# Performance work log

Measured on AMD Instinct MI355X. Metric: run time of the kernel, lower is better.

## Reference

```python
import jax, jax.numpy as jnp
import numpy as np

B, N, FIN, T = 4, 10000, 1, 12
K, CF, FT, H, NH = 3, 64, 64, 2, 4
E = 160000


def setup_inputs() -> dict:
    key = jax.random.key(0)
    ks = jax.random.split(key, 16)
    s = 0.05
    return {
        'x': jax.random.normal(ks[0], (B, N, FIN, T), jnp.float32),
        'edge_index': jax.random.randint(ks[1], (2, E), 0, N, jnp.int32),
        'cheb_w': jax.random.normal(ks[2], (K, CF, FIN), jnp.float32) * s,
        'cheb_b': jnp.zeros((CF,), jnp.float32),
        'gat_w': jax.random.normal(ks[3], (H * CF, CF), jnp.float32) * s,
        'att_src': jax.random.normal(ks[4], (H, CF), jnp.float32) * s,
        'att_dst': jax.random.normal(ks[5], (H, CF), jnp.float32) * s,
        'gat_b': jnp.zeros((CF,), jnp.float32),
        'tc_w': jax.random.normal(ks[6], (FT, CF, 1, 3), jnp.float32) * s,
        'tc_b': jnp.zeros((FT,), jnp.float32),
        'in_w': jax.random.normal(ks[7], (3 * FT, FT), jnp.float32) * s,
        'in_b': jnp.zeros((3 * FT,), jnp.float32),
        'out_w': jax.random.normal(ks[8], (FT, FT), jnp.float32) * s,
        'out_b': jnp.zeros((FT,), jnp.float32),
        'res_w': jax.random.normal(ks[9], (FT, FIN, 1, 1), jnp.float32) * s,
        'res_b': jnp.zeros((FT,), jnp.float32),
        'ln_g': jnp.ones((FT,), jnp.float32),
        'ln_b': jnp.zeros((FT,), jnp.float32),
        'bc_w': jax.random.normal(ks[10], (FT, CF, 1, 3), jnp.float32) * s,
        'bc_b': jnp.zeros((FT,), jnp.float32),
        'fc_w': jax.random.normal(ks[11], (FT, CF, 1, 3), jnp.float32) * s,
        'fc_b': jnp.zeros((FT,), jnp.float32),
    }


def conv1x3(inp, w, b):
    # Conv2d kernel (1,3), stride 1, pad (0,1) over (B,C,N,T): 1D conv along time.
    out = jax.lax.conv_general_dilated(inp, w, (1, 1), ((0, 0), (1, 1)),
                                       dimension_numbers=('NCHW', 'OIHW', 'NCHW'))
    return out + b[None, :, None, None]


def reference(x, edge_index, cheb_w, cheb_b, gat_w, att_src, att_dst, gat_b,
              tc_w, tc_b, in_w, in_b, out_w, out_b, res_w, res_b, ln_g, ln_b,
              bc_w, bc_b, fc_w, fc_b):
    Bx, Nx, Fin, Tt = x.shape
    BN = Bx * Nx
    src, dst = edge_index[0], edge_index[1]
    # ChebConv norm (PyG, lambda_max=2, sym): L_hat = -D^{-1/2} A D^{-1/2}, zero diag
    deg = jax.ops.segment_sum(jnp.ones_like(src, jnp.float32), src, num_segments=BN)
    dis = jnp.where(deg > 0, deg ** -0.5, 0.0)
    w_e = -dis[src] * dis[dst]
    loops = jnp.arange(BN, dtype=src.dtype)
    src_g = jnp.concatenate([src, loops])
    dst_g = jnp.concatenate([dst, loops])

    def prop(v):  # v: (BN, F) -> L_hat @ v
        return jax.ops.segment_sum(w_e[:, None] * v[src], dst, num_segments=BN)

    def spatial(xt):  # xt: (BN, Fin) -> (BN, CF); ChebConv then GAT (eval, no dropout)
        Tx0 = xt
        out = Tx0 @ cheb_w[0].T
        Tx1 = prop(Tx0)
        out = out + Tx1 @ cheb_w[1].T
        for kk in range(2, K):
            Tx2 = 2.0 * prop(Tx1) - Tx0
            out = out + Tx2 @ cheb_w[kk].T
            Tx0, Tx1 = Tx1, Tx2
        h = out + cheb_b
        # GATConv: heads=H, concat=False, self-loops added for all BN nodes
        xp = (h @ gat_w.T).reshape(BN, H, CF)
        a_s = (xp * att_src).sum(-1)  # (BN,H)
        a_d = (xp * att_dst).sum(-1)
        e = jax.nn.leaky_relu(a_s[src_g] + a_d[dst_g], 0.2)  # (E+BN,H)
        m = jax.ops.segment_max(e, dst_g, num_segments=BN)
        p = jnp.exp(e - m[dst_g])
        z = jax.ops.segment_sum(p, dst_g, num_segments=BN)
        alpha = p / z[dst_g]
        agg = jax.ops.segment_sum(alpha[:, :, None] * xp[src_g], dst_g, num_segments=BN)
        return agg.mean(1) + gat_b

    # batch graph convs across timesteps
    x_t = x.transpose(3, 0, 1, 2).reshape(Tt, BN, Fin)
    sp = jax.vmap(spatial)(x_t)  # (T,BN,CF)
    spatial_out = sp.reshape(Tt, Bx, Nx, CF).transpose(1, 3, 2, 0)  # (B,CF,N,T)

    tc = conv1x3(spatial_out, tc_w, tc_b)  # (B,FT,N,T)
    temp_in = tc.transpose(0, 2, 3, 1).reshape(BN, Tt, FT)
    # MultiheadAttention (batch_first, 4 heads, eval)
    qkv = temp_in @ in_w.T + in_b
    q, k, v = jnp.split(qkv, 3, axis=-1)
    dh = FT // NH
    q = q.reshape(BN, Tt, NH, dh)
    k = k.reshape(BN, Tt, NH, dh)
    v = v.reshape(BN, Tt, NH, dh)
    sc = jnp.einsum('bqhd,bkhd->bhqk', q, k) / jnp.sqrt(jnp.float32(dh))
    a = jax.nn.softmax(sc, axis=-1)
    o = jnp.einsum('bhqk,bkhd->bqhd', a, v).reshape(BN, Tt, FT)
    attn = o @ out_w.T + out_b
    temp_out = attn.reshape(Bx, Nx, Tt, FT).transpose(0, 1, 3, 2)  # (B,N,FT,T)

    # residual 1x1 conv (stride 1)
    x_res = jnp.einsum('bnft,of->bnot', x, res_w[:, :, 0, 0]) + res_b[None, None, :, None]
    zr = jax.nn.relu(x_res + temp_out)  # (B,N,FT,T)
    mu = zr.mean(axis=2, keepdims=True)
    var = ((zr - mu) ** 2).mean(axis=2, keepdims=True)
    result = (zr - mu) * jax.lax.rsqrt(var + 1e-5) * ln_g[None, None, :, None] + ln_b[None, None, :, None]

    rp = result.transpose(0, 2, 1, 3)  # (B,FT,N,T)
    backcast = conv1x3(rp, bc_w, bc_b).transpose(0, 2, 1, 3)
    forecast = conv1x3(rp, fc_w, fc_b).transpose(0, 2, 1, 3)
    return (backcast, forecast)
```

## Files before the change

kernel.cpp:

```cpp
#include <hip/hip_runtime.h>

#define BN 40000
#define TT 12
#define EE 160000

typedef __attribute__((ext_vector_type(4))) float f32x4;
typedef __attribute__((ext_vector_type(4))) short s16x4;
typedef __attribute__((ext_vector_type(8))) short s16x8;

__device__ __forceinline__ float lrelu(float v){ return v > 0.f ? v : 0.2f*v; }

__device__ __forceinline__ short bf(float f){
  union { float f; unsigned u; } x; x.f = f;
  unsigned r = x.u + 0x7fffu + ((x.u >> 16) & 1u);
  return (short)(r >> 16);
}

__device__ __forceinline__ unsigned cvtpk(float lo, float hi){
  unsigned r;
  asm("v_cvt_pk_bf16_f32 %0, %1, %2" : "=v"(r) : "v"(lo), "v"(hi));
  return r;
}

__global__ void k_histprep(const int* __restrict__ ei, int* __restrict__ degcnt, int* __restrict__ cnt,
                       const float* __restrict__ cheb_w, const float* __restrict__ cheb_b,
                       const float* __restrict__ gat_w, const float* __restrict__ att_src,
                       const float* __restrict__ att_dst, const float* __restrict__ gat_b,
                       const float* __restrict__ tc_w, const float* __restrict__ tc_b,
                       const float* __restrict__ in_w, const float* __restrict__ out_w,
                       const float* __restrict__ bc_w, const float* __restrict__ fc_w,
                       float* __restrict__ gwbuf, short* __restrict__ wp, float* __restrict__ btcT){
  if (blockIdx.x < 625){
    int e = blockIdx.x*256 + threadIdx.x;
    if (e < EE){
      atomicAdd(&degcnt[ei[e]], 1);
      atomicAdd(&cnt[ei[EE + e]], 1);
    }
    return;
  }
  if (blockIdx.x == 625){
    __shared__ float sgw[384]; __shared__ float sgc[128];
    int hc = threadIdx.x;
    if (hc < 128){
      for (int k=0;k<3;++k){
        float a=0; for (int c=0;c<64;++c) a += cheb_w[k*64+c]*gat_w[hc*64+c];
        sgw[k*128+hc]=a; gwbuf[k*128+hc]=a;
      }
      float g=0; for (int c=0;c<64;++c) g += cheb_b[c]*gat_w[hc*64+c];
      sgc[hc]=g; gwbuf[384+hc]=g;
    }
    __syncthreads();
    if (hc<6){ int k=hc>>1, h=hc&1; float a=0,d=0;
      for (int c=0;c<64;++c){ float g=sgw[k*128+h*64+c]; a+=g*att_src[h*64+c]; d+=g*att_dst[h*64+c]; }
      gwbuf[512+hc]=a; gwbuf[518+hc]=d; }
    if (hc<2){ float a=0,d=0;
      for (int c=0;c<64;++c){ float g=sgc[hc*64+c]; a+=g*att_src[hc*64+c]; d+=g*att_dst[hc*64+c]; }
      gwbuf[524+hc]=a; gwbuf[526+hc]=d; }
    __syncthreads();
    if (hc < 64){
      int o = hc;
      short* gw2 = wp + 46080;
      float sbias[3];
      for (int dt=0; dt<3; ++dt){
        float s[6] = {0,0,0,0,0,0};
        float sb = 0.f;
        for (int c=0;c<64;++c){
          float wv = tc_w[o*192 + c*3 + dt];
          for (int j=0;j<3;++j){
            s[j]   += wv * sgw[j*128 + c];
            s[3+j] += wv * sgw[j*128 + 64 + c];
          }
          sb += wv * (gat_b[c] + 0.5f*(sgc[c] + sgc[64+c]));
        }
        for (int j=0;j<6;++j) gw2[o*40 + dt*6 + j] = bf(s[j]);
        sbias[dt] = sb;
      }
      for (int k=18;k<40;++k) gw2[o*40+k] = 0;
      for (int t=0;t<16;++t){
        float b = tc_b[o];
        if (t < 12){
          if (t > 0)  b += sbias[0];
          b += sbias[1];
          if (t < 11) b += sbias[2];
        }
        btcT[o*16+t] = b;
      }
    }
    return;
  }
  int i = (blockIdx.x-626)*256 + threadIdx.x;
  if (i >= 46080) return;
  float v;
  if (i < 13824){ int j=i/72, k=i%72; v = (k<64)? in_w[j*64+k] : 0.f; }
  else if (i < 27648){ int d=i-13824; int dt=d/4608, rr=d%4608, o=rr/72, c=rr%72; v = (c<64)? bc_w[o*192+c*3+dt] : 0.f; }
  else if (i < 41472){ int d=i-27648; int dt=d/4608, rr=d%4608, o=rr/72, c=rr%72; v = (c<64)? fc_w[o*192+c*3+dt] : 0.f; }
  else               { int d=i-41472; int o=d/72, c=d%72; v = (c<64)? out_w[o*64+c] : 0.f; }
  wp[i] = bf(v);
}

__global__ void k_scanA(const int* __restrict__ cnt, int* __restrict__ bsum,
                        const short* __restrict__ wp, short* __restrict__ wp2){
  if (blockIdx.x >= 157){
    int i = (blockIdx.x-157)*256 + threadIdx.x;
    if (i >= 40960) return;
    int f2 = i >> 9, lane = (i >> 3) & 63, e = i & 7;
    int l15 = lane & 15, l4 = lane >> 4;
    int src;
    if (f2 < 24){
      int grp = f2 >> 3, nt = (f2 >> 1) & 3, kc = f2 & 1;
      src = 0     + ((grp*4+nt)*16 + l15)*72 + kc*32 + l4*8 + e;
    } else if (f2 < 32){
      int g = f2 - 24; int mt = g >> 1, kc = g & 1;
      src = 41472 + (mt*16 + l15)*72 + kc*32 + l4*8 + e;
    } else if (f2 < 56){
      int g = f2 - 32; int dt = g >> 3, kc = (g >> 2) & 1, nt = g & 3;
      src = 13824 + (dt*64 + nt*16 + l15)*72 + kc*32 + l4*8 + e;
    } else {
      int g = f2 - 56; int dt = g >> 3, kc = (g >> 2) & 1, nt = g & 3;
      src = 27648 + (dt*64 + nt*16 + l15)*72 + kc*32 + l4*8 + e;
    }
    wp2[i] = wp[src];
    return;
  }
  __shared__ int s[256];
  int i = blockIdx.x*256 + threadIdx.x;
  int v = (i < BN) ? cnt[i] : 0;
  s[threadIdx.x] = v; __syncthreads();
  for (int off=128; off>0; off>>=1){
    if (threadIdx.x < off) s[threadIdx.x] += s[threadIdx.x+off];
    __syncthreads();
  }
  if (threadIdx.x == 0) bsum[blockIdx.x] = s[0];
}

__global__ void k_scanB(const int* __restrict__ bsum, int* __restrict__ bbase, int* __restrict__ rowptr){
  __shared__ int s[256];
  int tid = threadIdx.x;
  int v = (tid < 157) ? bsum[tid] : 0;
  s[tid] = v; __syncthreads();
  for (int off=1; off<256; off<<=1){
    int t = (tid>=off) ? s[tid-off] : 0;
    __syncthreads();
    s[tid] += t;
    __syncthreads();
  }
  if (tid < 157) bbase[tid] = s[tid] - v;
  if (tid == 0) rowptr[BN] = EE;
}

__global__ void k_scanC(const int* __restrict__ cnt, const int* __restrict__ bbase,
                        int* __restrict__ rowptr, int* __restrict__ cursor){
  __shared__ int s[256];
  int i = blockIdx.x*256 + threadIdx.x;
  int v = (i < BN) ? cnt[i] : 0;
  s[threadIdx.x] = v; __syncthreads();
  for (int off=1; off<256; off<<=1){
    int t = (threadIdx.x>=off) ? s[threadIdx.x-off] : 0;
    __syncthreads();
    s[threadIdx.x] += t;
    __syncthreads();
  }
  if (i < BN){
    int r = bbase[blockIdx.x] + s[threadIdx.x] - v;
    rowptr[i] = r; cursor[i] = r;
  }
}

__global__ void k_scatter(const int* __restrict__ ei, const int* __restrict__ degcnt,
                          int* __restrict__ cursor, int* __restrict__ esrc, float* __restrict__ ew){
  int e = blockIdx.x*256 + threadIdx.x;
  if (e < EE){
    int s = ei[e], d = ei[EE+e];
    int p = atomicAdd(&cursor[d], 1);
    esrc[p] = s;
    int ds_ = degcnt[s], dd_ = degcnt[d];
    float isd = ds_ > 0 ? rsqrtf((float)ds_) : 0.f;
    float idd = dd_ > 0 ? rsqrtf((float)dd_) : 0.f;
    ew[p] = -isd*idd;
  }
}

__global__ void k_prop1v(const float* __restrict__ x, const int* __restrict__ rowptr,
                         const int* __restrict__ esrc, const float* __restrict__ ew,
                         float* __restrict__ tx1){
  int i = blockIdx.x*256 + threadIdx.x;
  if (i >= BN*3) return;
  int d = i/3, q = i - d*3;
  int r0 = rowptr[d], r1 = rowptr[d+1];
  float4 a = {0.f,0.f,0.f,0.f};
  for (int p=r0;p<r1;++p){
    float wv = ew[p];
    float4 v = ((const float4*)x)[esrc[p]*3 + q];
    a.x += wv*v.x; a.y += wv*v.y; a.z += wv*v.z; a.w += wv*v.w;
  }
  ((float4*)tx1)[i] = a;
}

__global__ void k_prop2v(const float* __restrict__ x, const float* __restrict__ tx1,
                         const int* __restrict__ rowptr, const int* __restrict__ esrc,
                         const float* __restrict__ ew, float* __restrict__ tx2){
  int i = blockIdx.x*256 + threadIdx.x;
  if (i >= BN*3) return;
  int d = i/3, q = i - d*3;
  int r0 = rowptr[d], r1 = rowptr[d+1];
  float4 a = {0.f,0.f,0.f,0.f};
  for (int p=r0;p<r1;++p){
    float wv = ew[p];
    float4 v = ((const float4*)tx1)[esrc[p]*3 + q];
    a.x += wv*v.x; a.y += wv*v.y; a.z += wv*v.z; a.w += wv*v.w;
  }
  float4 xv = ((const float4*)x)[i];
  float4 o; o.x = 2.f*a.x - xv.x; o.y = 2.f*a.y - xv.y; o.z = 2.f*a.z - xv.z; o.w = 2.f*a.w - xv.w;
  ((float4*)tx2)[i] = o;
}

__global__ __launch_bounds__(256) void k_gat4(const float* __restrict__ x, const float* __restrict__ tx1,
     const float* __restrict__ tx2, const int* __restrict__ rowptr, const int* __restrict__ esrc,
     const float* __restrict__ gwbuf, float* __restrict__ coef, int cst){
  int i = blockIdx.x*256 + threadIdx.x;
  if (i >= BN*3) return;
  int d = i/3, q = i - d*3;

  float as[2][3], ad[2][3], asc[2], adc[2];
  #pragma unroll
  for (int h=0;h<2;++h){
    #pragma unroll
    for (int k=0;k<3;++k){ as[h][k] = gwbuf[512+2*k+h]; ad[h][k] = gwbuf[518+2*k+h]; }
    asc[h] = gwbuf[524+h]; adc[h] = gwbuf[526+h];
  }

  float4 t0 = ((const float4*)x)[d*3+q];
  float4 t1 = ((const float4*)tx1)[d*3+q];
  float4 t2 = ((const float4*)tx2)[d*3+q];
  float td0[4] = {t0.x,t0.y,t0.z,t0.w};
  float td1[4] = {t1.x,t1.y,t1.z,t1.w};
  float td2[4] = {t2.x,t2.y,t2.z,t2.w};

  float adh[2][4], S0[2][4], S1[2][4], S2[2][4], Z[2][4];
  #pragma unroll
  for (int h=0;h<2;++h){
    #pragma unroll
    for (int t=0;t<4;++t){
      adh[h][t] = td0[t]*ad[h][0] + td1[t]*ad[h][1] + td2[t]*ad[h][2] + adc[h];
      float es = lrelu(td0[t]*as[h][0] + td1[t]*as[h][1] + td2[t]*as[h][2] + asc[h] + adh[h][t]);
      float p = __expf(es);
      S0[h][t] = p*td0[t]; S1[h][t] = p*td1[t]; S2[h][t] = p*td2[t]; Z[h][t] = p;
    }
  }
  int r0 = rowptr[d], r1 = rowptr[d+1];
  for (int p=r0;p<r1;++p){
    int s = esrc[p];
    float4 v0 = ((const float4*)x)[s*3+q];
    float4 v1 = ((const float4*)tx1)[s*3+q];
    float4 v2 = ((const float4*)tx2)[s*3+q];
    float s0[4] = {v0.x,v0.y,v0.z,v0.w};
    float s1[4] = {v1.x,v1.y,v1.z,v1.w};
    float s2[4] = {v2.x,v2.y,v2.z,v2.w};
    #pragma unroll
    for (int h=0;h<2;++h){
      #pragma unroll
      for (int t=0;t<4;++t){
        float e = lrelu(s0[t]*as[h][0] + s1[t]*as[h][1] + s2[t]*as[h][2] + asc[h] + adh[h][t]);
        float pp = __expf(e);
        S0[h][t] += pp*s0[t]; S1[h][t] += pp*s1[t]; S2[h][t] += pp*s2[t]; Z[h][t] += pp;
      }
    }
  }
  float* cw = coef + (size_t)d*cst + q*32;
  #pragma unroll
  for (int t=0;t<4;++t){
    float inv0 = 0.5f/Z[0][t], inv1 = 0.5f/Z[1][t];
    float4 w4; w4.x = S0[0][t]*inv0; w4.y = S1[0][t]*inv0; w4.z = S2[0][t]*inv0; w4.w = S0[1][t]*inv1;
    *(float4*)(cw + t*8) = w4;
    float2 w2; w2.x = S1[1][t]*inv1; w2.y = S2[1][t]*inv1;
    *(float2*)(cw + t*8 + 4) = w2;
  }
}

__global__ __launch_bounds__(448) void k_temporal9(
  const float* __restrict__ coef, int cst, const float* __restrict__ x,
  const short* __restrict__ wp, const short* __restrict__ wp2, const float* __restrict__ btcT,
  const float* __restrict__ in_b, const float* __restrict__ out_b,
  const float* __restrict__ res_w, const float* __restrict__ res_b,
  const float* __restrict__ ln_g, const float* __restrict__ ln_b,
  const float* __restrict__ bc_b, const float* __restrict__ fc_b,
  float* __restrict__ out)
{
  __shared__ __align__(16) short lds[26880];

  const int tid = threadIdx.x;
  const int wv = tid >> 6;
  const int lane = tid & 63;
  const int l15 = lane & 15, l4 = lane >> 4;
  const int nd = blockIdx.x*7 + wv;
  if (nd >= BN) return;

  short* nb  = lds + wv*3840;
  short* tcO = nb;
  short* K   = nb + 1152;
  short* R   = nb + 1152;
  short* Vt  = nb + 2304;
  short* Pb  = nb + 3328;
  short* Pb2 = nb + 3584;

  const f32x4 z4 = {0.f,0.f,0.f,0.f};
  s16x8 zf;
  #pragma unroll
  for (int j=0;j<8;++j) zf[j]=0;

  s16x8 aA;
  {
    const float* cb = coef + (size_t)nd*cst;
    float av[8];
    #pragma unroll
    for (int e=0; e<8; ++e){
      int k = l4*8 + e;
      float v = 0.f;
      if (k < 18){
        int dt = (k>=12) ? 2 : ((k>=6) ? 1 : 0);
        int j = k - dt*6;
        int u = l15 - 1 + dt;
        if (u >= 0 && u < 12) v = cb[u*8 + j];
      }
      av[e] = v;
    }
    unsigned* ap = (unsigned*)&aA;
    ap[0]=cvtpk(av[0],av[1]); ap[1]=cvtpk(av[2],av[3]);
    ap[2]=cvtpk(av[4],av[5]); ap[3]=cvtpk(av[6],av[7]);
  }

  {
    #pragma unroll
    for (int nt=0; nt<4; ++nt){
      s16x8 b = *(const s16x8*)&wp[46080 + (nt*16+l15)*40 + l4*8];
      f32x4 acc = __builtin_amdgcn_mfma_f32_16x16x32_bf16(aA, b, z4, 0,0,0);
      float4 bb = *(const float4*)&btcT[(nt*16+l15)*16 + l4*4];
      unsigned p01 = cvtpk(acc[0]+bb.x, acc[1]+bb.y);
      unsigned p23 = cvtpk(acc[2]+bb.z, acc[3]+bb.w);
      int c = nt*16 + l15, rb = l4*4;
      tcO[(rb+0)*72+c] = (short)p01; tcO[(rb+1)*72+c] = (short)(p01>>16);
      tcO[(rb+2)*72+c] = (short)p23; tcO[(rb+3)*72+c] = (short)(p23>>16);
    }
  }

  {
    s16x8 a0 = *(const s16x8*)&tcO[l15*72 +  0 + l4*8];
    s16x8 a1 = *(const s16x8*)&tcO[l15*72 + 32 + l4*8];
    #pragma unroll
    for (int grp=0; grp<3; ++grp){
      f32x4 acc[4];
      #pragma unroll
      for (int nt=0; nt<4; ++nt){
        s16x8 b0 = *(const s16x8*)&wp2[(((grp*8 + nt*2 + 0)*64 + lane))*8];
        acc[nt] = __builtin_amdgcn_mfma_f32_16x16x32_bf16(a0, b0, z4, 0,0,0);
        s16x8 b1 = *(const s16x8*)&wp2[(((grp*8 + nt*2 + 1)*64 + lane))*8];
        acc[nt] = __builtin_amdgcn_mfma_f32_16x16x32_bf16(a1, b1, acc[nt], 0,0,0);
      }
      #pragma unroll
      for (int nt=0; nt<4; ++nt){
        float bb = in_b[(grp*4+nt)*16 + l15];
        unsigned p01 = cvtpk(acc[nt][0]+bb, acc[nt][1]+bb);
        unsigned p23 = cvtpk(acc[nt][2]+bb, acc[nt][3]+bb);
        if (grp==0){
          int c = nt*16+l15, rb = l4*4;
          tcO[(rb+0)*72+c] = (short)p01; tcO[(rb+1)*72+c] = (short)(p01>>16);
          tcO[(rb+2)*72+c] = (short)p23; tcO[(rb+3)*72+c] = (short)(p23>>16);
        } else if (grp==1){
          int c = nt*16+l15, rb = l4*4;
          K[(rb+0)*72+c] = (short)p01; K[(rb+1)*72+c] = (short)(p01>>16);
          K[(rb+2)*72+c] = (short)p23; K[(rb+3)*72+c] = (short)(p23>>16);
        } else {
          int2 pk2; pk2.x = (int)p01; pk2.y = (int)p23;
          *(int2*)&Vt[(nt*16 + l15)*16 + l4*4] = pk2;
        }
      }
    }
  }

  {
    #pragma unroll 1
    for (int hp=0; hp<2; ++hp){
      const int h0 = hp*2, h1 = hp*2 + 1;
      s16x8 qa0 = zf, kb0 = zf, qa1 = zf, kb1 = zf;
      if (l4 < 2){
        qa0 = *(const s16x8*)&tcO[l15*72 + h0*16 + l4*8];
        kb0 = *(const s16x8*)&K[l15*72 + h0*16 + l4*8];
        qa1 = *(const s16x8*)&tcO[l15*72 + h1*16 + l4*8];
        kb1 = *(const s16x8*)&K[l15*72 + h1*16 + l4*8];
      }
      f32x4 sc0 = __builtin_amdgcn_mfma_f32_16x16x32_bf16(qa0, kb0, z4, 0,0,0);
      f32x4 sc1 = __builtin_amdgcn_mfma_f32_16x16x32_bf16(qa1, kb1, z4, 0,0,0);
      float invz0[4], invz1[4], ev0[4], ev1[4];
      #pragma unroll
      for (int r=0; r<4; ++r){
        float e0 = (l15 < 12) ? __expf(sc0[r]*0.25f) : 0.f;
        float e1 = (l15 < 12) ? __expf(sc1[r]*0.25f) : 0.f;
        float z0 = e0, z1 = e1;
        #pragma unroll
        for (int dd=1; dd<16; dd<<=1){ z0 += __shfl_xor(z0, dd); z1 += __shfl_xor(z1, dd); }
        invz0[r] = 1.f/z0; invz1[r] = 1.f/z1;
        ev0[r] = e0; ev1[r] = e1;
      }
      {
        unsigned a01 = cvtpk(ev0[0],ev0[1]), a23 = cvtpk(ev0[2],ev0[3]);
        unsigned b01 = cvtpk(ev1[0],ev1[1]), b23 = cvtpk(ev1[2],ev1[3]);
        int rb = l4*4, c = l15;
        Pb [(rb+0)*16+c] = (short)a01; Pb [(rb+1)*16+c] = (short)(a01>>16);
        Pb [(rb+2)*16+c] = (short)a23; Pb [(rb+3)*16+c] = (short)(a23>>16);
        Pb2[(rb+0)*16+c] = (short)b01; Pb2[(rb+1)*16+c] = (short)(b01>>16);
        Pb2[(rb+2)*16+c] = (short)b23; Pb2[(rb+3)*16+c] = (short)(b23>>16);
      }
      s16x8 pa0 = zf, vb0 = zf, pa1 = zf, vb1 = zf;
      if (l4 < 2){
        pa0 = *(const s16x8*)&Pb [l15*16 + l4*8];
        vb0 = *(const s16x8*)&Vt[(h0*16 + l15)*16 + l4*8];
        pa1 = *(const s16x8*)&Pb2[l15*16 + l4*8];
        vb1 = *(const s16x8*)&Vt[(h1*16 + l15)*16 + l4*8];
      }
      f32x4 ov0 = __builtin_amdgcn_mfma_f32_16x16x32_bf16(pa0, vb0, z4, 0,0,0);
      f32x4 ov1 = __builtin_amdgcn_mfma_f32_16x16x32_bf16(pa1, vb1, z4, 0,0,0);
      {
        unsigned a01 = cvtpk(ov0[0]*invz0[0], ov0[1]*invz0[1]);
        unsigned a23 = cvtpk(ov0[2]*invz0[2], ov0[3]*invz0[3]);
        unsigned b01 = cvtpk(ov1[0]*invz1[0], ov1[1]*invz1[1]);
        unsigned b23 = cvtpk(ov1[2]*invz1[2], ov1[3]*invz1[3]);
        int c0 = h0*16 + l15, c1 = h1*16 + l15, rb = l4*4;
        tcO[(rb+0)*72+c0] = (short)a01; tcO[(rb+1)*72+c0] = (short)(a01>>16);
        tcO[(rb+2)*72+c0] = (short)a23; tcO[(rb+3)*72+c0] = (short)(a23>>16);
        tcO[(rb+0)*72+c1] = (short)b01; tcO[(rb+1)*72+c1] = (short)(b01>>16);
        tcO[(rb+2)*72+c1] = (short)b23; tcO[(rb+3)*72+c1] = (short)(b23>>16);
      }
    }
  }

  {
    s16x4 zz; zz[0]=0; zz[1]=0; zz[2]=0; zz[3]=0;
    for (int i=lane; i<108; i+=64){
      int rr = i/18, cc = i%18;
      int row = (rr==0) ? 0 : (12 + rr);
      *(s16x4*)&R[row*72 + cc*4] = zz;
    }
    s16x8 a0 = *(const s16x8*)&tcO[l15*72 +  0 + l4*8];
    s16x8 a1 = *(const s16x8*)&tcO[l15*72 + 32 + l4*8];
    f32x4 acc[4];
    #pragma unroll
    for (int nt=0; nt<4; ++nt){
      s16x8 w0 = *(const s16x8*)&wp2[(((24 + nt*2 + 0)*64 + lane))*8];
      acc[nt] = __builtin_amdgcn_mfma_f32_16x16x32_bf16(a0, w0, z4, 0,0,0);
      s16x8 w1 = *(const s16x8*)&wp2[(((24 + nt*2 + 1)*64 + lane))*8];
      acc[nt] = __builtin_amdgcn_mfma_f32_16x16x32_bf16(a1, w1, acc[nt], 0,0,0);
    }
    float4 xv = {0.f,0.f,0.f,0.f};
    if (l4 < 3) xv = *(const float4*)&x[(size_t)nd*12 + l4*4];
    float xr[4] = {xv.x, xv.y, xv.z, xv.w};
    float zr[4][4], sum[4]={0,0,0,0}, sq[4]={0,0,0,0};
    #pragma unroll
    for (int nt=0; nt<4; ++nt){
      int o = nt*16 + l15;
      float ob=out_b[o], rw=res_w[o], rb2=res_b[o];
      #pragma unroll
      for (int r=0; r<4; ++r){
        float v = acc[nt][r] + ob + xr[r]*rw + rb2;
        v = v>0.f ? v : 0.f;
        zr[nt][r]=v; sum[r]+=v; sq[r]+=v*v;
      }
    }
    #pragma unroll
    for (int r=0; r<4; ++r){
      #pragma unroll
      for (int dd=1; dd<16; dd<<=1){ sum[r]+=__shfl_xor(sum[r],dd); sq[r]+=__shfl_xor(sq[r],dd); }
    }
    if (l4 < 3){
      float mu4[4], iv4[4];
      #pragma unroll
      for (int r=0; r<4; ++r){
        float mu = sum[r]*(1.f/64.f);
        float va = sq[r]*(1.f/64.f) - mu*mu;
        mu4[r] = mu; iv4[r] = rsqrtf(fmaxf(va,0.f) + 1e-5f);
      }
      #pragma unroll
      for (int nt=0; nt<4; ++nt){
        int o = nt*16 + l15;
        float g = ln_g[o], b2 = ln_b[o];
        float r0 = (zr[nt][0]-mu4[0])*iv4[0]*g + b2;
        float r1 = (zr[nt][1]-mu4[1])*iv4[1]*g + b2;
        float r2 = (zr[nt][2]-mu4[2])*iv4[2]*g + b2;
        float r3 = (zr[nt][3]-mu4[3])*iv4[3]*g + b2;
        unsigned p01 = cvtpk(r0,r1), p23 = cvtpk(r2,r3);
        int rb = l4*4;
        R[(rb+1)*72+o] = (short)p01; R[(rb+2)*72+o] = (short)(p01>>16);
        R[(rb+3)*72+o] = (short)p23; R[(rb+4)*72+o] = (short)(p23>>16);
      }
    }
  }

  {
    f32x4 aB[4] = {z4,z4,z4,z4};
    f32x4 aF[4] = {z4,z4,z4,z4};
    #pragma unroll
    for (int dt=0; dt<3; ++dt){
      #pragma unroll
      for (int kc=0; kc<2; ++kc){
        s16x8 ar = *(const s16x8*)&R[(l15 + dt)*72 + kc*32 + l4*8];
        #pragma unroll
        for (int nt=0; nt<4; ++nt){
          s16x8 wb = *(const s16x8*)&wp2[16384 + (((dt*8 + kc*4 + nt)*64 + lane))*8];
          aB[nt] = __builtin_amdgcn_mfma_f32_16x16x32_bf16(ar, wb, aB[nt], 0,0,0);
          s16x8 wf = *(const s16x8*)&wp2[28672 + (((dt*8 + kc*4 + nt)*64 + lane))*8];
          aF[nt] = __builtin_amdgcn_mfma_f32_16x16x32_bf16(ar, wf, aF[nt], 0,0,0);
        }
      }
    }
    if (l4 < 3){
      #pragma unroll
      for (int nt=0; nt<4; ++nt){
        int o = nt*16 + l15;
        float bb = bc_b[o], fb = fc_b[o];
        float4 v; v.x=aB[nt][0]+bb; v.y=aB[nt][1]+bb; v.z=aB[nt][2]+bb; v.w=aB[nt][3]+bb;
        *(float4*)&out[(size_t)nd*768 + o*12 + l4*4] = v;
        float4 f; f.x=aF[nt][0]+fb; f.y=aF[nt][1]+fb; f.z=aF[nt][2]+fb; f.w=aF[nt][3]+fb;
        *(float4*)&out[30720000 + (size_t)nd*768 + o*12 + l4*4] = f;
      }
    }
  }
}

extern "C" void kernel_launch(void* const* d_in, const int* in_sizes, int n_in,
                              void* d_out, int out_size, void* d_ws, size_t ws_size,
                              hipStream_t stream){
  const float* x      = (const float*)d_in[0];
  const int*   ei     = (const int*)d_in[1];
  const float* cheb_w = (const float*)d_in[2];
  const float* cheb_b = (const float*)d_in[3];
  const float* gat_w  = (const float*)d_in[4];
  const float* att_src= (const float*)d_in[5];
  const float* att_dst= (const float*)d_in[6];
  const float* gat_b  = (const float*)d_in[7];
  const float* tc_w   = (const float*)d_in[8];
  const float* tc_b   = (const float*)d_in[9];
  const float* in_w   = (const float*)d_in[10];
  const float* in_b   = (const float*)d_in[11];
  const float* out_w  = (const float*)d_in[12];
  const float* out_b  = (const float*)d_in[13];
  const float* res_w  = (const float*)d_in[14];
  const float* res_b  = (const float*)d_in[15];
  const float* ln_g   = (const float*)d_in[16];
  const float* ln_b   = (const float*)d_in[17];
  const float* bc_w   = (const float*)d_in[18];
  const float* bc_b   = (const float*)d_in[19];
  const float* fc_w   = (const float*)d_in[20];
  const float* fc_b   = (const float*)d_in[21];
  float* out = (float*)d_out;

  char* w = (char*)d_ws;
  size_t off = 0;
  auto alloc = [&](size_t bytes)->void*{ void* p = w + off; off += (bytes + 255) & ~(size_t)255; return p; };
  int*   cnt2   = (int*)alloc((size_t)2*BN*4);
  int*   degcnt = cnt2;
  int*   cnt    = cnt2 + BN;
  int*   rowptr = (int*)alloc((size_t)(BN+1)*4);
  int*   cursor = (int*)alloc((size_t)BN*4);
  int*   esrc   = (int*)alloc((size_t)EE*4);
  float* ew     = (float*)alloc((size_t)EE*4);
  float* tx1    = (float*)alloc((size_t)BN*TT*4);
  float* tx2    = (float*)alloc((size_t)BN*TT*4);
  float* gwb    = (float*)alloc(1024*4);
  short* wpack  = (short*)alloc((size_t)48640*2);
  short* wpack2 = (short*)alloc((size_t)40960*2);
  float* btcT   = (float*)alloc(1024*4);
  int*   bsum   = (int*)alloc(157*4);
  int*   bbase  = (int*)alloc(157*4);

  size_t coefBytes = (size_t)BN*TT*8*4;
  float* coefp; int cst;
  if (off + coefBytes <= ws_size){ coefp = (float*)(w + off); off += coefBytes; cst = 96; }
  else { coefp = out; cst = 768; }

  hipMemsetAsync(cnt2, 0, (size_t)2*BN*4, stream);
  k_histprep<<<806, 256, 0, stream>>>(ei, degcnt, cnt, cheb_w, cheb_b, gat_w, att_src, att_dst,
                                      gat_b, tc_w, tc_b, in_w, out_w, bc_w, fc_w, gwb, wpack, btcT);
  k_scanA   <<<317, 256, 0, stream>>>(cnt, bsum, wpack, wpack2);
  k_scanB   <<<1, 256, 0, stream>>>(bsum, bbase, rowptr);
  k_scanC   <<<157, 256, 0, stream>>>(cnt, bbase, rowptr, cursor);
  k_scatter <<<(EE+255)/256, 256, 0, stream>>>(ei, degcnt, cursor, esrc, ew);
  k_prop1v  <<<(BN*3+255)/256, 256, 0, stream>>>(x, rowptr, esrc, ew, tx1);
  k_prop2v  <<<(BN*3+255)/256, 256, 0, stream>>>(x, tx1, rowptr, esrc, ew, tx2);
  k_gat4    <<<(BN*3+255)/256, 256, 0, stream>>>(x, tx1, tx2, rowptr, esrc, gwb, coefp, cst);
  k_temporal9<<<(BN+6)/7, 448, 0, stream>>>(coefp, cst, x, wpack, wpack2, btcT, in_b, out_b,
                                            res_w, res_b, ln_g, ln_b, bc_b, fc_b, out);
}
```

Baseline: 266.1 us.

## Fold temporal conv into QKV projection and interleave Chebyshev features for gather

Precomputes the product of the in_proj weights with the folded GAT/temporal-conv weights (and the matching biases) in the prep block, so the temporal kernel computes Q/K/V with a single K=32 MFMA per tile instead of a conv followed by a two-step K=64 projection. It also packs x, Tx1 and Tx2 into one interleaved 48-byte record per node-quarter, so each neighbor gather in the GAT kernel reads one contiguous record instead of three separate arrays. In exchange, one prep block does more serial work, weight rounding to bf16 now happens after the fold, and the propagation kernel writes a larger packed buffer.

Result: slower. 306.3 us (+15.1%).

```diff
diff --git a/kernel.cpp b/kernel.cpp
--- a/kernel.cpp
+++ b/kernel.cpp
@@ -27,9 +27,10 @@
                        const float* __restrict__ gat_w, const float* __restrict__ att_src,
                        const float* __restrict__ att_dst, const float* __restrict__ gat_b,
                        const float* __restrict__ tc_w, const float* __restrict__ tc_b,
-                       const float* __restrict__ in_w, const float* __restrict__ out_w,
+                       const float* __restrict__ in_w, const float* __restrict__ in_b,
+                       const float* __restrict__ out_w,
                        const float* __restrict__ bc_w, const float* __restrict__ fc_w,
-                       float* __restrict__ gwbuf, short* __restrict__ wp, float* __restrict__ btcT){
+                       float* __restrict__ gwbuf, short* __restrict__ wp, float* __restrict__ bbT){
   if (blockIdx.x < 625){
     int e = blockIdx.x*256 + threadIdx.x;
     if (e < EE){
@@ -40,6 +41,7 @@
   }
   if (blockIdx.x == 625){
     __shared__ float sgw[384]; __shared__ float sgc[128];
+    __shared__ float gwtcF[64*18]; __shared__ float btcF[16*64];
     int hc = threadIdx.x;
     if (hc < 128){
       for (int k=0;k<3;++k){
@@ -72,7 +74,10 @@
           }
           sb += wv * (gat_b[c] + 0.5f*(sgc[c] + sgc[64+c]));
         }
-        for (int j=0;j<6;++j) gw2[o*40 + dt*6 + j] = bf(s[j]);
+        for (int j=0;j<6;++j){
+          gw2[o*40 + dt*6 + j] = bf(s[j]);
+          gwtcF[o*18 + dt*6 + j] = s[j];
+        }
         sbias[dt] = sb;
       }
       for (int k=18;k<40;++k) gw2[o*40+k] = 0;
@@ -83,7 +88,25 @@
           b += sbias[1];
           if (t < 11) b += sbias[2];
         }
-        btcT[o*16+t] = b;
+        btcF[t*64+o] = b;
+      }
+    }
+    __syncthreads();
+    if (hc < 192){
+      int j = hc;
+      float wrow[64];
+      for (int o=0;o<64;++o) wrow[o] = in_w[j*64+o];
+      short* wbq = wp + 48640;
+      for (int k=0;k<18;++k){
+        float a = 0.f;
+        for (int o=0;o<64;++o) a += wrow[o]*gwtcF[o*18+k];
+        wbq[j*32+k] = bf(a);
+      }
+      for (int k=18;k<32;++k) wbq[j*32+k] = 0;
+      for (int t=0;t<16;++t){
+        float a = in_b[j];
+        for (int o=0;o<64;++o) a += wrow[o]*btcF[t*64+o];
+        bbT[j*16+t] = a;
       }
     }
     return;
@@ -196,9 +219,9 @@
   ((float4*)tx1)[i] = a;
 }
 
-__global__ void k_prop2v(const float* __restrict__ x, const float* __restrict__ tx1,
+__global__ void k_prop2p(const float* __restrict__ x, const float* __restrict__ tx1,
                          const int* __restrict__ rowptr, const int* __restrict__ esrc,
-                         const float* __restrict__ ew, float* __restrict__ tx2){
+                         const float* __restrict__ ew, float* __restrict__ pk){
   int i = blockIdx.x*256 + threadIdx.x;
   if (i >= BN*3) return;
   int d = i/3, q = i - d*3;
@@ -210,12 +233,16 @@
     a.x += wv*v.x; a.y += wv*v.y; a.z += wv*v.z; a.w += wv*v.w;
   }
   float4 xv = ((const float4*)x)[i];
+  float4 t1o = ((const float4*)tx1)[i];
   float4 o; o.x = 2.f*a.x - xv.x; o.y = 2.f*a.y - xv.y; o.z = 2.f*a.z - xv.z; o.w = 2.f*a.w - xv.w;
-  ((float4*)tx2)[i] = o;
-}
-
-__global__ __launch_bounds__(256) void k_gat4(const float* __restrict__ x, const float* __restrict__ tx1,
-     const float* __restrict__ tx2, const int* __restrict__ rowptr, const int* __restrict__ esrc,
+  float* base = pk + (size_t)i*12;
+  *(float4*)(base+0) = xv;
+  *(float4*)(base+4) = t1o;
+  *(float4*)(base+8) = o;
+}
+
+__global__ __launch_bounds__(256) void k_gat5(const float* __restrict__ pk,
+     const int* __restrict__ rowptr, const int* __restrict__ esrc,
      const float* __restrict__ gwbuf, float* __restrict__ coef, int cst){
   int i = blockIdx.x*256 + threadIdx.x;
   if (i >= BN*3) return;
@@ -229,9 +256,10 @@
     asc[h] = gwbuf[524+h]; adc[h] = gwbuf[526+h];
   }
 
-  float4 t0 = ((const float4*)x)[d*3+q];
-  float4 t1 = ((const float4*)tx1)[d*3+q];
-  float4 t2 = ((const float4*)tx2)[d*3+q];
+  const float* bd = pk + (size_t)i*12;
+  float4 t0 = *(const float4*)(bd+0);
+  float4 t1 = *(const float4*)(bd+4);
+  float4 t2 = *(const float4*)(bd+8);
   float td0[4] = {t0.x,t0.y,t0.z,t0.w};
   float td1[4] = {t1.x,t1.y,t1.z,t1.w};
   float td2[4] = {t2.x,t2.y,t2.z,t2.w};
@@ -250,9 +278,10 @@
   int r0 = rowptr[d], r1 = rowptr[d+1];
   for (int p=r0;p<r1;++p){
     int s = esrc[p];
-    float4 v0 = ((const float4*)x)[s*3+q];
-    float4 v1 = ((const float4*)tx1)[s*3+q];
-    float4 v2 = ((const float4*)tx2)[s*3+q];
+    const float* bs = pk + (size_t)(s*3+q)*12;
+    float4 v0 = *(const float4*)(bs+0);
+    float4 v1 = *(const float4*)(bs+4);
+    float4 v2 = *(const float4*)(bs+8);
     float s0[4] = {v0.x,v0.y,v0.z,v0.w};
     float s1[4] = {v1.x,v1.y,v1.z,v1.w};
     float s2[4] = {v2.x,v2.y,v2.z,v2.w};
@@ -277,11 +306,10 @@
   }
 }
 
-__global__ __launch_bounds__(448) void k_temporal9(
+__global__ __launch_bounds__(448) void k_temporalA(
   const float* __restrict__ coef, int cst, const float* __restrict__ x,
-  const short* __restrict__ wp, const short* __restrict__ wp2, const float* __restrict__ btcT,
-  const float* __restrict__ in_b, const float* __restrict__ out_b,
-  const float* __restrict__ res_w, const float* __restrict__ res_b,
+  const short* __restrict__ wp, const short* __restrict__ wp2, const float* __restrict__ bbT,
+  const float* __restrict__ out_b, const float* __restrict__ res_w, const float* __restrict__ res_b,
   const float* __restrict__ ln_g, const float* __restrict__ ln_b,
   const float* __restrict__ bc_b, const float* __restrict__ fc_b,
   float* __restrict__ out)
@@ -332,48 +360,35 @@
   {
     #pragma unroll
     for (int nt=0; nt<4; ++nt){
-      s16x8 b = *(const s16x8*)&wp[46080 + (nt*16+l15)*40 + l4*8];
+      s16x8 b = *(const s16x8*)&wp[48640 + (nt*16+l15)*32 + l4*8];
       f32x4 acc = __builtin_amdgcn_mfma_f32_16x16x32_bf16(aA, b, z4, 0,0,0);
-      float4 bb = *(const float4*)&btcT[(nt*16+l15)*16 + l4*4];
+      float4 bb = *(const float4*)&bbT[(nt*16+l15)*16 + l4*4];
       unsigned p01 = cvtpk(acc[0]+bb.x, acc[1]+bb.y);
       unsigned p23 = cvtpk(acc[2]+bb.z, acc[3]+bb.w);
       int c = nt*16 + l15, rb = l4*4;
       tcO[(rb+0)*72+c] = (short)p01; tcO[(rb+1)*72+c] = (short)(p01>>16);
       tcO[(rb+2)*72+c] = (short)p23; tcO[(rb+3)*72+c] = (short)(p23>>16);
     }
-  }
-
-  {
-    s16x8 a0 = *(const s16x8*)&tcO[l15*72 +  0 + l4*8];
-    s16x8 a1 = *(const s16x8*)&tcO[l15*72 + 32 + l4*8];
-    #pragma unroll
-    for (int grp=0; grp<3; ++grp){
-      f32x4 acc[4];
-      #pragma unroll
-      for (int nt=0; nt<4; ++nt){
-        s16x8 b0 = *(const s16x8*)&wp2[(((grp*8 + nt*2 + 0)*64 + lane))*8];
-        acc[nt] = __builtin_amdgcn_mfma_f32_16x16x32_bf16(a0, b0, z4, 0,0,0);
-        s16x8 b1 = *(const s16x8*)&wp2[(((grp*8 + nt*2 + 1)*64 + lane))*8];
-        acc[nt] = __builtin_amdgcn_mfma_f32_16x16x32_bf16(a1, b1, acc[nt], 0,0,0);
-      }
-      #pragma unroll
-      for (int nt=0; nt<4; ++nt){
-        float bb = in_b[(grp*4+nt)*16 + l15];
-        unsigned p01 = cvtpk(acc[nt][0]+bb, acc[nt][1]+bb);
-        unsigned p23 = cvtpk(acc[nt][2]+bb, acc[nt][3]+bb);
-        if (grp==0){
-          int c = nt*16+l15, rb = l4*4;
-          tcO[(rb+0)*72+c] = (short)p01; tcO[(rb+1)*72+c] = (short)(p01>>16);
-          tcO[(rb+2)*72+c] = (short)p23; tcO[(rb+3)*72+c] = (short)(p23>>16);
-        } else if (grp==1){
-          int c = nt*16+l15, rb = l4*4;
-          K[(rb+0)*72+c] = (short)p01; K[(rb+1)*72+c] = (short)(p01>>16);
-          K[(rb+2)*72+c] = (short)p23; K[(rb+3)*72+c] = (short)(p23>>16);
-        } else {
-          int2 pk2; pk2.x = (int)p01; pk2.y = (int)p23;
-          *(int2*)&Vt[(nt*16 + l15)*16 + l4*4] = pk2;
-        }
-      }
+    #pragma unroll
+    for (int nt=4; nt<8; ++nt){
+      s16x8 b = *(const s16x8*)&wp[48640 + (nt*16+l15)*32 + l4*8];
+      f32x4 acc = __builtin_amdgcn_mfma_f32_16x16x32_bf16(aA, b, z4, 0,0,0);
+      float4 bb = *(const float4*)&bbT[(nt*16+l15)*16 + l4*4];
+      unsigned p01 = cvtpk(acc[0]+bb.x, acc[1]+bb.y);
+      unsigned p23 = cvtpk(acc[2]+bb.z, acc[3]+bb.w);
+      int c = (nt-4)*16 + l15, rb = l4*4;
+      K[(rb+0)*72+c] = (short)p01; K[(rb+1)*72+c] = (short)(p01>>16);
+      K[(rb+2)*72+c] = (short)p23; K[(rb+3)*72+c] = (short)(p23>>16);
+    }
+    #pragma unroll
+    for (int nt=8; nt<12; ++nt){
+      s16x8 b = *(const s16x8*)&wp[48640 + (nt*16+l15)*32 + l4*8];
+      f32x4 acc = __builtin_amdgcn_mfma_f32_16x16x32_bf16(aA, b, z4, 0,0,0);
+      float4 bb = *(const float4*)&bbT[(nt*16+l15)*16 + l4*4];
+      unsigned p01 = cvtpk(acc[0]+bb.x, acc[1]+bb.y);
+      unsigned p23 = cvtpk(acc[2]+bb.z, acc[3]+bb.w);
+      int2 pk2; pk2.x = (int)p01; pk2.y = (int)p23;
+      *(int2*)&Vt[((nt-8)*16 + l15)*16 + l4*4] = pk2;
     }
   }
 
@@ -563,11 +578,11 @@
   int*   esrc   = (int*)alloc((size_t)EE*4);
   float* ew     = (float*)alloc((size_t)EE*4);
   float* tx1    = (float*)alloc((size_t)BN*TT*4);
-  float* tx2    = (float*)alloc((size_t)BN*TT*4);
+  float* pk     = (float*)alloc((size_t)BN*3*12*4);
   float* gwb    = (float*)alloc(1024*4);
-  short* wpack  = (short*)alloc((size_t)48640*2);
+  short* wpack  = (short*)alloc((size_t)54784*2);
   short* wpack2 = (short*)alloc((size_t)40960*2);
-  float* btcT   = (float*)alloc(1024*4);
+  float* bbT    = (float*)alloc((size_t)192*16*4);
   int*   bsum   = (int*)alloc(157*4);
   int*   bbase  = (int*)alloc(157*4);
 
@@ -578,14 +593,15 @@
 
   hipMemsetAsync(cnt2, 0, (size_t)2*BN*4, stream);
   k_histprep<<<806, 256, 0, stream>>>(ei, degcnt, cnt, cheb_w, cheb_b, gat_w, att_src, att_dst,
-                                      gat_b, tc_w, tc_b, in_w, out_w, bc_w, fc_w, gwb, wpack, btcT);
+                                      gat_b, tc_w, tc_b, in_w, in_b, out_w, bc_w, fc_w,
+                                      gwb, wpack, bbT);
   k_scanA   <<<317, 256, 0, stream>>>(cnt, bsum, wpack, wpack2);
   k_scanB   <<<1, 256, 0, stream>>>(bsum, bbase, rowptr);
   k_scanC   <<<157, 256, 0, stream>>>(cnt, bbase, rowptr, cursor);
   k_scatter <<<(EE+255)/256, 256, 0, stream>>>(ei, degcnt, cursor, esrc, ew);
   k_prop1v  <<<(BN*3+255)/256, 256, 0, stream>>>(x, rowptr, esrc, ew, tx1);
-  k_prop2v  <<<(BN*3+255)/256, 256, 0, stream>>>(x, tx1, rowptr, esrc, ew, tx2);
-  k_gat4    <<<(BN*3+255)/256, 256, 0, stream>>>(x, tx1, tx2, rowptr, esrc, gwb, coefp, cst);
-  k_temporal9<<<(BN+6)/7, 448, 0, stream>>>(coefp, cst, x, wpack, wpack2, btcT, in_b, out_b,
+  k_prop2p  <<<(BN*3+255)/256, 256, 0, stream>>>(x, tx1, rowptr, esrc, ew, pk);
+  k_gat5    <<<(BN*3+255)/256, 256, 0, stream>>>(pk, rowptr, esrc, gwb, coefp, cst);
+  k_temporalA<<<(BN+6)/7, 448, 0, stream>>>(coefp, cst, x, wpack, wpack2, bbT, out_b,
                                             res_w, res_b, ln_g, ln_b, bc_b, fc_b, out);
 }
```
